# Kernel tuning notes

Measured on AMD Instinct MI355X. Metric: run time of the kernel, lower is better.

Reference implementation:

```python
import jax, jax.numpy as jnp
import numpy as np

BN_EPS = 1e-5
NN_CHUNK = 1024  # unknown points processed per distance-matrix tile


def _batch_ids(cnt, total):
    # contiguous per-batch layout -> batch id of each point via cumsum/searchsorted
    return jnp.searchsorted(jnp.cumsum(cnt), jnp.arange(total), side='right')


def three_nn(unknown, known, ub_id, kb_id):
    """Ragged brute-force 3-NN. Returns (squared dists [N,3], global idx [N,3])."""
    N = unknown.shape[0]
    nchunk = N // NN_CHUNK
    u = unknown.reshape(nchunk, NN_CHUNK, 3)
    ub = ub_id.reshape(nchunk, NN_CHUNK)

    def body(args):
        uc, bc = args
        d2 = jnp.sum((uc[:, None, :] - known[None, :, :]) ** 2, axis=-1)  # [chunk, M]
        d2 = jnp.where(bc[:, None] == kb_id[None, :], d2, jnp.inf)  # mask cross-batch pairs
        neg_d, idx = jax.lax.top_k(-d2, 3)
        return -neg_d, idx

    d2, idx = jax.lax.map(body, (u, ub))
    return d2.reshape(N, 3), idx.reshape(N, 3)


def three_interpolate(known_feats, idx, weight):
    # gather [N,3,C] then inverse-distance weighted sum -> [N,C]
    gathered = known_feats[idx]  # [N,3,C]
    return jnp.einsum('nkc,nk->nc', gathered, weight)


def conv_bn_relu(x, W, gamma, beta):
    # 1x1 Conv2d over [1,C,N,1] == pointwise matmul; BN (training stats) over points
    h = x @ W.T  # [N, C_out]
    mean = jnp.mean(h, axis=0)
    var = jnp.mean((h - mean) ** 2, axis=0)  # biased, as torch BN normalization
    h = (h - mean) * jax.lax.rsqrt(var + BN_EPS) * gamma + beta
    return jax.nn.relu(h)


def setup_inputs() -> dict:
    key = jax.random.key(0)
    ks = jax.random.split(key, 10)
    B, Nper, Mper, C1, C2 = 4, 16384, 4096, 128, 256
    N, M = B * Nper, B * Mper
    unknown = jax.random.normal(ks[0], (N, 3), jnp.float32) * 10.0
    known = jax.random.normal(ks[1], (M, 3), jnp.float32) * 10.0
    unknown_feats = jax.random.normal(ks[2], (N, C1), jnp.float32)
    known_feats = jax.random.normal(ks[3], (M, C2), jnp.float32)
    unknown_batch_cnt = jnp.full((B,), Nper, jnp.int32)
    known_batch_cnt = jnp.full((B,), Mper, jnp.int32)
    Cin = C1 + C2  # 384
    W1 = jax.random.normal(ks[4], (256, Cin), jnp.float32) * (1.0 / np.sqrt(Cin))
    W2 = jax.random.normal(ks[5], (256, 256), jnp.float32) * (1.0 / np.sqrt(256))
    g1 = jnp.ones((256,), jnp.float32); b1 = jnp.zeros((256,), jnp.float32)
    g2 = jnp.ones((256,), jnp.float32); b2 = jnp.zeros((256,), jnp.float32)
    return {"unknown": unknown, "unknown_batch_cnt": unknown_batch_cnt,
            "known": known, "known_batch_cnt": known_batch_cnt,
            "unknown_feats": unknown_feats, "known_feats": known_feats,
            "W1": W1, "g1": g1, "b1": b1, "W2": W2, "g2": g2, "b2": b2}


def reference(unknown, unknown_batch_cnt, known, known_batch_cnt,
              unknown_feats, known_feats, W1, g1, b1, W2, g2, b2):
    ub_id = _batch_ids(unknown_batch_cnt, unknown.shape[0])
    kb_id = _batch_ids(known_batch_cnt, known.shape[0])
    dist, idx = three_nn(unknown, known, ub_id, kb_id)  # squared dists, as CUDA kernel
    dist_recip = 1.0 / (dist + 1e-8)
    weight = dist_recip / jnp.sum(dist_recip, axis=-1, keepdims=True)
    interpolated = three_interpolate(known_feats, idx, weight)  # [N, C2]
    new_features = jnp.concatenate([interpolated, unknown_feats], axis=1)  # [N, C2+C1]
    new_features = conv_bn_relu(new_features, W1, g1, b1)
    new_features = conv_bn_relu(new_features, W2, g2, b2)
    return new_features  # [N, 256]
```

## Files before the change

kernel.cpp:

```cpp
#include <hip/hip_runtime.h>
#include <math.h>

typedef __attribute__((ext_vector_type(8))) short short8;
typedef __attribute__((ext_vector_type(4))) float f32x4;

#define INF 3.0e38f
#define BN_EPS 1e-5f

#define NB 1024
#define XMIN (-64.0f)
#define BW 0.125f
#define INVW 8.0f
#define PA 192

__device__ __forceinline__ unsigned short f2bf(float x) {
    union { float f; unsigned u; } v; v.f = x;
    unsigned r = v.u + 0x7FFF + ((v.u >> 16) & 1);
    return (unsigned short)(r >> 16);
}
__device__ __forceinline__ float bf2f(unsigned short u) {
    return __uint_as_float(((unsigned)u) << 16);
}
__device__ __forceinline__ unsigned long long shflx_u64(unsigned long long v, int m) {
    int lo = __shfl_xor((int)(unsigned)(v & 0xFFFFFFFFULL), m, 64);
    int hi = __shfl_xor((int)(unsigned)(v >> 32), m, 64);
    return ((unsigned long long)(unsigned)hi << 32) | (unsigned)lo;
}

__global__ __launch_bounds__(256) void hist2_kernel(
    const float* __restrict__ kn, const int* __restrict__ kcnt, int M,
    const float* __restrict__ un, const int* __restrict__ ucnt, int N,
    int B, int* __restrict__ kc, int* __restrict__ qc)
{
    int j = blockIdx.x * 256 + threadIdx.x;
    const float* P; const int* C; int* out; int idx;
    if (j < M) { P = kn; C = kcnt; out = kc; idx = j; }
    else { idx = j - M; if (idx >= N) return; P = un; C = ucnt; out = qc; }
    int cum = 0, bb = 0;
    for (int i = 0; i < B; i++) { int c = C[i]; if (idx >= cum) bb = i; cum += c; }
    float x = P[idx * 3];
    int bi = (int)((x - XMIN) * INVW);
    bi = min(max(bi, 0), NB - 1);
    atomicAdd(&out[bb * NB + bi], 1);
}

__global__ __launch_bounds__(1024) void scan2_kernel(
    const int* __restrict__ kc, int* __restrict__ kbs, int* __restrict__ kcur,
    const int* __restrict__ qc, int* __restrict__ qbs, int* __restrict__ qcur,
    int T)
{
    __shared__ int ts[1024];
    const int* cnt = blockIdx.x ? qc : kc;
    int* bs  = blockIdx.x ? qbs : kbs;
    int* cur = blockIdx.x ? qcur : kcur;

    int tid = threadIdx.x;
    int base = tid * 4;
    int v0 = 0, v1 = 0, v2 = 0, v3 = 0;
    if (base + 0 < T) v0 = cnt[base + 0];
    if (base + 1 < T) v1 = cnt[base + 1];
    if (base + 2 < T) v2 = cnt[base + 2];
    if (base + 3 < T) v3 = cnt[base + 3];
    int s = v0 + v1 + v2 + v3;
    ts[tid] = s;
    __syncthreads();
    for (int off = 1; off < 1024; off <<= 1) {
        int t = (tid >= off) ? ts[tid - off] : 0;
        __syncthreads();
        ts[tid] += t;
        __syncthreads();
    }
    int ex = ts[tid] - s;
    if (base + 0 < T) { bs[base + 0] = ex; cur[base + 0] = ex; } ex += v0;
    if (base + 1 < T) { bs[base + 1] = ex; cur[base + 1] = ex; } ex += v1;
    if (base + 2 < T) { bs[base + 2] = ex; cur[base + 2] = ex; } ex += v2;
    if (base + 3 < T) { bs[base + 3] = ex; cur[base + 3] = ex; } ex += v3;
    if (tid == ((T - 1) >> 2)) bs[T] = ts[tid];
}

__global__ __launch_bounds__(256) void scatter2_kernel(
    const float* __restrict__ kn, const int* __restrict__ kcnt, int M,
    const float* __restrict__ un, const int* __restrict__ ucnt, int N,
    int B, int* __restrict__ kcur, float4* __restrict__ kscat,
    int* __restrict__ qcur, float4* __restrict__ qscat)
{
    int j = blockIdx.x * 256 + threadIdx.x;
    const float* P; const int* C; int* cur; float4* out; int idx;
    if (j < M) { P = kn; C = kcnt; cur = kcur; out = kscat; idx = j; }
    else { idx = j - M; if (idx >= N) return; P = un; C = ucnt; cur = qcur; out = qscat; }
    int cum = 0, bb = 0;
    for (int i = 0; i < B; i++) { int c = C[i]; if (idx >= cum) bb = i; cum += c; }
    float x = P[idx * 3], y = P[idx * 3 + 1], z = P[idx * 3 + 2];
    int bi = (int)((x - XMIN) * INVW);
    bi = min(max(bi, 0), NB - 1);
    int pos = atomicAdd(&cur[bb * NB + bi], 1);
    out[pos] = make_float4(x, y, z, __int_as_float(idx));
}

__global__ __launch_bounds__(256) void knn4_kernel(
    const int* __restrict__ ucnt, const int* __restrict__ kbs,
    const float4* __restrict__ qscat, const float4* __restrict__ scat,
    int B, float* __restrict__ wgt, int* __restrict__ idxo)
{
    int tid = threadIdx.x;
    int wv = tid >> 6;
    int lane = tid & 63;
    int qi = lane & 15;
    int r4 = lane >> 4;
    int pbase = blockIdx.x * 64;
    int qpos = pbase + wv * 16 + qi;

    int cum = 0, bb = 0;
    for (int i = 0; i < B; i++) { int c = ucnt[i]; if (pbase >= cum) bb = i; cum += c; }

    float4 qf = qscat[qpos];
    float ux = qf.x, uy = qf.y, uz = qf.z;

    int kst = kbs[bb * NB];
    int ken = kbs[bb * NB + NB];

    int bq = (int)((ux - XMIN) * INVW);
    bq = min(max(bq, 0), NB - 1);
    int sp = kbs[bb * NB + bq];

    int abase = sp - PA / 2;
    if (abase + PA > ken) abase = ken - PA;
    if (abase < kst) abase = kst;
    int aend = min(abase + PA, ken);

    float d0 = INF, d1 = INF, d2v = INF;
    auto upd = [&](float e) {
        float m0 = fmaxf(e, d0), m1 = fmaxf(e, d1);
        d0 = fminf(e, d0); d1 = fminf(m0, d1); d2v = fminf(m1, d2v);
    };
    {
        int alo = abase + r4 * (PA / 4);
        int ahi = min(alo + PA / 4, aend);
        int i = alo;
        for (; i + 4 <= ahi; i += 4) {
            float e[4];
#pragma unroll
            for (int c = 0; c < 4; c++) {
                float4 f = scat[i + c];
                float dx = f.x - ux, dy = f.y - uy, dz = f.z - uz;
                e[c] = __builtin_fmaf(dx, dx, __builtin_fmaf(dy, dy, dz * dz));
            }
#pragma unroll
            for (int c = 0; c < 4; c++) upd(e[c]);
        }
        for (; i < ahi; i++) {
            float4 f = scat[i];
            float dx = f.x - ux, dy = f.y - uy, dz = f.z - uz;
            upd(__builtin_fmaf(dx, dx, __builtin_fmaf(dy, dy, dz * dz)));
        }
    }
#pragma unroll
    for (int s = 16; s <= 32; s <<= 1) {
        float e0 = __shfl_xor(d0, s, 64);
        float e1 = __shfl_xor(d1, s, 64);
        float e2 = __shfl_xor(d2v, s, 64);
        upd(e0); upd(e1); upd(e2);
    }
    float thr = d2v;

    float Wr = fminf(sqrtf(thr), 300.0f);
    int blo = max((int)((ux - Wr - XMIN) * INVW) - 1, 0);
    int bhi = min((int)((ux + Wr - XMIN) * INVW) + 1, NB - 1);
    int pLo = kbs[bb * NB + blo];
    int pHi = kbs[bb * NB + bhi + 1];
    int n = pHi - pLo;
    int quar = (n + 3) >> 2;
    int mylo = pLo + r4 * quar;
    int myhi = min(mylo + quar, pHi);

    unsigned long long k0 = ~0ULL, k1 = ~0ULL, k2 = ~0ULL;
    auto insK = [&](unsigned long long k) {
        bool cc0 = k < k0;
        unsigned long long t0 = cc0 ? k : k0;
        unsigned long long t1 = cc0 ? k0 : k;
        bool cc1 = t1 < k1;
        unsigned long long u0 = cc1 ? t1 : k1;
        unsigned long long u1 = cc1 ? k1 : t1;
        k0 = t0; k1 = u0;
        k2 = u1 < k2 ? u1 : k2;
    };

    int i = mylo;
    for (; i + 4 <= myhi; i += 4) {
        float e[4]; int ix[4];
#pragma unroll
        for (int c = 0; c < 4; c++) {
            float4 f = scat[i + c];
            float dx = f.x - ux, dy = f.y - uy, dz = f.z - uz;
            e[c] = __builtin_fmaf(dx, dx, __builtin_fmaf(dy, dy, dz * dz));
            ix[c] = __float_as_int(f.w);
        }
        float m4 = fminf(fminf(e[0], e[1]), fminf(e[2], e[3]));
        if (m4 <= thr) {
#pragma unroll
            for (int c = 0; c < 4; c++) {
                if (e[c] <= thr) {
                    insK(((unsigned long long)__float_as_uint(e[c]) << 32) |
                         (unsigned)ix[c]);
                    thr = fminf(thr, __uint_as_float((unsigned)(k2 >> 32)));
                }
            }
        }
    }
    for (; i < myhi; i++) {
        float4 f = scat[i];
        float dx = f.x - ux, dy = f.y - uy, dz = f.z - uz;
        float e = __builtin_fmaf(dx, dx, __builtin_fmaf(dy, dy, dz * dz));
        if (e <= thr) {
            insK(((unsigned long long)__float_as_uint(e) << 32) |
                 (unsigned)__float_as_int(f.w));
            thr = fminf(thr, __uint_as_float((unsigned)(k2 >> 32)));
        }
    }

#pragma unroll
    for (int s = 16; s <= 32; s <<= 1) {
        unsigned long long e0 = shflx_u64(k0, s);
        unsigned long long e1 = shflx_u64(k1, s);
        unsigned long long e2 = shflx_u64(k2, s);
        insK(e0); insK(e1); insK(e2);
    }

    if (r4 == 0) {
        float dd0 = __uint_as_float((unsigned)(k0 >> 32));
        float dd1 = __uint_as_float((unsigned)(k1 >> 32));
        float dd2 = __uint_as_float((unsigned)(k2 >> 32));
        float r0 = 1.0f / (dd0 + 1e-8f);
        float r1 = 1.0f / (dd1 + 1e-8f);
        float r2 = 1.0f / (dd2 + 1e-8f);
        float rs = 1.0f / (r0 + r1 + r2);
        int orig = __float_as_int(qf.w);
        wgt[orig * 3 + 0] = r0 * rs;
        wgt[orig * 3 + 1] = r1 * rs;
        wgt[orig * 3 + 2] = r2 * rs;
        idxo[orig * 3 + 0] = (int)(unsigned)k0;
        idxo[orig * 3 + 1] = (int)(unsigned)k1;
        idxo[orig * 3 + 2] = (int)(unsigned)k2;
    }
}

__global__ __launch_bounds__(256) void wconv_kernel(
    const float* __restrict__ W1, const float* __restrict__ W2,
    unsigned short* __restrict__ W1b, unsigned short* __restrict__ W2b,
    int n1, int n2)
{
    int i = blockIdx.x * 256 + threadIdx.x;
    if (i < n1) W1b[i] = f2bf(W1[i]);
    int j = i - n1;
    if (j >= 0 && j < n2) W2b[j] = f2bf(W2[j]);
}

template <int K, int MODE>
__global__ __launch_bounds__(256) void gemm_bf16_kernel(
    const void* __restrict__ Aa, const float* __restrict__ ufeat,
    const unsigned short* __restrict__ W,
    const float* __restrict__ wgt, const int* __restrict__ idxv,
    const float* __restrict__ bnsum, const float* __restrict__ bnsq,
    const float* __restrict__ bng, const float* __restrict__ bnb, float invN,
    void* __restrict__ Cv, float* __restrict__ gsum, float* __restrict__ gsq)
{
    __shared__ unsigned short As[128 * 40];
    __shared__ unsigned short Bs[128 * 40];
    __shared__ float colsum[128];
    __shared__ float colsq[128];
    __shared__ float sc[256], sh[256];

    int tid = threadIdx.x;
    int w = tid >> 6, lane = tid & 63;
    int r = w >> 1, cq = w & 1;
    int m16 = lane & 15, q = lane >> 4;
    int bm = blockIdx.x * 128, bn = blockIdx.y * 128;

    if (MODE == 1) {
        float mean = bnsum[tid] * invN;
        float var = bnsq[tid] * invN - mean * mean;
        float scv = bng[tid] * rsqrtf(var + BN_EPS);
        sc[tid] = scv;
        sh[tid] = bnb[tid] - mean * scv;
    }

    int srow = tid >> 2;
    int kc = (tid & 3) * 8;
    float w0a[2], w1a[2], w2a[2];
    int j0a[2], j1a[2], j2a[2];
    if (MODE == 2) {
#pragma unroll
        for (int t = 0; t < 2; t++) {
            int pp = bm + srow + 64 * t;
            w0a[t] = wgt[pp * 3 + 0]; w1a[t] = wgt[pp * 3 + 1]; w2a[t] = wgt[pp * 3 + 2];
            j0a[t] = idxv[pp * 3 + 0]; j1a[t] = idxv[pp * 3 + 1]; j2a[t] = idxv[pp * 3 + 2];
        }
    }

    f32x4 acc[4][4];
#pragma unroll
    for (int i = 0; i < 4; i++)
#pragma unroll
        for (int j = 0; j < 4; j++) acc[i][j] = (f32x4){0.f, 0.f, 0.f, 0.f};

#pragma unroll
    for (int k0 = 0; k0 < K; k0 += 32) {
        __syncthreads();
#pragma unroll
        for (int t = 0; t < 2; t++) {
            int row = srow + 64 * t;
            int c = k0 + kc;
            ushort4 o0, o1;
            if (MODE == 2) {
                if (c < 256) {
                    const float* f0 = (const float*)Aa + (size_t)j0a[t] * 256 + c;
                    const float* f1 = (const float*)Aa + (size_t)j1a[t] * 256 + c;
                    const float* f2 = (const float*)Aa + (size_t)j2a[t] * 256 + c;
                    float4 x0 = *(const float4*)f0, x1 = *(const float4*)(f0 + 4);
                    float4 y0 = *(const float4*)f1, y1 = *(const float4*)(f1 + 4);
                    float4 z0 = *(const float4*)f2, z1 = *(const float4*)(f2 + 4);
                    float W0 = w0a[t], W1 = w1a[t], W2 = w2a[t];
                    o0.x = f2bf(x0.x * W0 + y0.x * W1 + z0.x * W2);
                    o0.y = f2bf(x0.y * W0 + y0.y * W1 + z0.y * W2);
                    o0.z = f2bf(x0.z * W0 + y0.z * W1 + z0.z * W2);
                    o0.w = f2bf(x0.w * W0 + y0.w * W1 + z0.w * W2);
                    o1.x = f2bf(x1.x * W0 + y1.x * W1 + z1.x * W2);
                    o1.y = f2bf(x1.y * W0 + y1.y * W1 + z1.y * W2);
                    o1.z = f2bf(x1.z * W0 + y1.z * W1 + z1.z * W2);
                    o1.w = f2bf(x1.w * W0 + y1.w * W1 + z1.w * W2);
                } else {
                    const float* fu = ufeat + (size_t)(bm + row) * 128 + (c - 256);
                    float4 u0 = *(const float4*)fu, u1 = *(const float4*)(fu + 4);
                    o0.x = f2bf(u0.x); o0.y = f2bf(u0.y);
                    o0.z = f2bf(u0.z); o0.w = f2bf(u0.w);
                    o1.x = f2bf(u1.x); o1.y = f2bf(u1.y);
                    o1.z = f2bf(u1.z); o1.w = f2bf(u1.w);
                }
            } else {
                const unsigned short* Ab = (const unsigned short*)Aa;
                ushort4 h0 = *(const ushort4*)(Ab + (size_t)(bm + row) * K + c);
                ushort4 h1v = *(const ushort4*)(Ab + (size_t)(bm + row) * K + c + 4);
                float4 s0 = *(const float4*)&sc[c];
                float4 s1 = *(const float4*)&sc[c + 4];
                float4 t0 = *(const float4*)&sh[c];
                float4 t1 = *(const float4*)&sh[c + 4];
                o0.x = f2bf(fmaxf(bf2f(h0.x) * s0.x + t0.x, 0.f));
                o0.y = f2bf(fmaxf(bf2f(h0.y) * s0.y + t0.y, 0.f));
                o0.z = f2bf(fmaxf(bf2f(h0.z) * s0.z + t0.z, 0.f));
                o0.w = f2bf(fmaxf(bf2f(h0.w) * s0.w + t0.w, 0.f));
                o1.x = f2bf(fmaxf(bf2f(h1v.x) * s1.x + t1.x, 0.f));
                o1.y = f2bf(fmaxf(bf2f(h1v.y) * s1.y + t1.y, 0.f));
                o1.z = f2bf(fmaxf(bf2f(h1v.z) * s1.z + t1.z, 0.f));
                o1.w = f2bf(fmaxf(bf2f(h1v.w) * s1.w + t1.w, 0.f));
            }
            *(ushort4*)&As[row * 40 + kc] = o0;
            *(ushort4*)&As[row * 40 + kc + 4] = o1;
            *(short8*)&Bs[row * 40 + kc] =
                *(const short8*)(W + (size_t)(bn + row) * K + k0 + kc);
        }
        __syncthreads();

        short8 af[4], bf[4];
#pragma unroll
        for (int sub = 0; sub < 4; sub++) {
            af[sub] = *(const short8*)&As[(r * 64 + sub * 16 + m16) * 40 + q * 8];
            bf[sub] = *(const short8*)&Bs[(cq * 64 + sub * 16 + m16) * 40 + q * 8];
        }
#pragma unroll
        for (int sm = 0; sm < 4; sm++)
#pragma unroll
            for (int sn = 0; sn < 4; sn++)
                acc[sm][sn] = __builtin_amdgcn_mfma_f32_16x16x32_bf16(
                    af[sm], bf[sn], acc[sm][sn], 0, 0, 0);
    }

    int row0 = bm + r * 64 + q * 4;
    int col0 = bn + cq * 64 + m16;
#pragma unroll
    for (int sm = 0; sm < 4; sm++)
#pragma unroll
        for (int sn = 0; sn < 4; sn++) {
            f32x4 v = acc[sm][sn];
#pragma unroll
            for (int reg = 0; reg < 4; reg++) {
                size_t idx = (size_t)(row0 + sm * 16 + reg) * 256 + col0 + sn * 16;
                if (MODE == 2) ((unsigned short*)Cv)[idx] = f2bf(v[reg]);
                else           ((float*)Cv)[idx] = v[reg];
            }
        }

    __syncthreads();
    if (tid < 128) { colsum[tid] = 0.f; colsq[tid] = 0.f; }
    __syncthreads();
#pragma unroll
    for (int sn = 0; sn < 4; sn++) {
        float sacc = 0.f, qacc = 0.f;
#pragma unroll
        for (int sm = 0; sm < 4; sm++) {
            f32x4 v = acc[sm][sn];
#pragma unroll
            for (int reg = 0; reg < 4; reg++) {
                sacc += v[reg];
                qacc += v[reg] * v[reg];
            }
        }
        int lc = cq * 64 + sn * 16 + m16;
        atomicAdd(&colsum[lc], sacc);
        atomicAdd(&colsq[lc], qacc);
    }
    __syncthreads();
    if (tid < 128) {
        atomicAdd(&gsum[bn + tid], colsum[tid]);
        atomicAdd(&gsq[bn + tid], colsq[tid]);
    }
}

__global__ __launch_bounds__(256) void final_act_kernel(
    const float* __restrict__ h2, const float* __restrict__ bnsum,
    const float* __restrict__ bnsq, const float* __restrict__ bng,
    const float* __restrict__ bnb, float invN,
    float* __restrict__ out, int total4)
{
    __shared__ float sc[256], sh[256];
    int c = threadIdx.x;
    float mean = bnsum[c] * invN;
    float var = bnsq[c] * invN - mean * mean;
    float scv = bng[c] * rsqrtf(var + BN_EPS);
    sc[c] = scv;
    sh[c] = bnb[c] - mean * scv;
    __syncthreads();

    int i = blockIdx.x * 256 + threadIdx.x;
    if (i >= total4) return;
    int c4 = i & 63;
    float4 v = ((const float4*)h2)[i];
    float4 s = *(const float4*)&sc[c4 * 4];
    float4 t = *(const float4*)&sh[c4 * 4];
    float4 o;
    o.x = fmaxf(v.x * s.x + t.x, 0.0f);
    o.y = fmaxf(v.y * s.y + t.y, 0.0f);
    o.z = fmaxf(v.z * s.z + t.z, 0.0f);
    o.w = fmaxf(v.w * s.w + t.w, 0.0f);
    ((float4*)out)[i] = o;
}

extern "C" void kernel_launch(void* const* d_in, const int* in_sizes, int n_in,
                              void* d_out, int out_size, void* d_ws, size_t ws_size,
                              hipStream_t stream)
{
    const float* unknown = (const float*)d_in[0];
    const int*   ucnt    = (const int*)d_in[1];
    const float* known   = (const float*)d_in[2];
    const int*   kcnt    = (const int*)d_in[3];
    const float* ufeat   = (const float*)d_in[4];
    const float* kfeat   = (const float*)d_in[5];
    const float* W1      = (const float*)d_in[6];
    const float* g1      = (const float*)d_in[7];
    const float* b1      = (const float*)d_in[8];
    const float* W2      = (const float*)d_in[9];
    const float* g2      = (const float*)d_in[10];
    const float* b2      = (const float*)d_in[11];

    int N = in_sizes[0] / 3;
    int B = in_sizes[1];
    int M = in_sizes[2] / 3;
    int T = B * NB;

    char* ws = (char*)d_ws;
    size_t off = 0;
    float* wgt = (float*)(ws + off);            off += (size_t)N * 3 * 4;
    int*   idxb = (int*)(ws + off);             off += (size_t)N * 3 * 4;
    float* stats = (float*)(ws + off);          off += 4 * 256 * 4;
    float* sum1 = stats,        *sq1 = stats + 256;
    float* sum2 = stats + 512,  *sq2 = stats + 768;
    int* kch = (int*)(ws + off);                off += (size_t)T * 4;
    int* qch = (int*)(ws + off);                off += (size_t)T * 4;
    int* kbs = (int*)(ws + off);                off += ((size_t)T + 1) * 4;
    int* qbs = (int*)(ws + off);                off += ((size_t)T + 1) * 4;
    int* kcur = (int*)(ws + off);               off += (size_t)T * 4;
    int* qcur = (int*)(ws + off);               off += (size_t)T * 4;
    unsigned short* W1b = (unsigned short*)(ws + off);  off += 256 * 384 * 2;
    unsigned short* W2b = (unsigned short*)(ws + off);  off += 256 * 256 * 2;
    off = (off + 255) & ~(size_t)255;
    float4* kscat = (float4*)(ws + off);        off += (size_t)M * sizeof(float4);
    float4* qscat = (float4*)(ws + off);        off += (size_t)N * sizeof(float4);
    off = (off + 255) & ~(size_t)255;
    unsigned short* h1 = (unsigned short*)(ws + off);   off += (size_t)N * 256 * 2;
    off = (off + 255) & ~(size_t)255;
    float* h2 = (float*)(ws + off);

    float invN = 1.0f / (float)N;

    hipMemsetAsync(stats, 0, 4 * 256 * 4 + 2 * (size_t)T * 4, stream);

    wconv_kernel<<<(256 * 384 + 256 * 256 + 255) / 256, 256, 0, stream>>>(
        W1, W2, W1b, W2b, 256 * 384, 256 * 256);

    hist2_kernel<<<(M + N + 255) / 256, 256, 0, stream>>>(
        known, kcnt, M, unknown, ucnt, N, B, kch, qch);
    scan2_kernel<<<2, 1024, 0, stream>>>(kch, kbs, kcur, qch, qbs, qcur, T);
    scatter2_kernel<<<(M + N + 255) / 256, 256, 0, stream>>>(
        known, kcnt, M, unknown, ucnt, N, B, kcur, kscat, qcur, qscat);
    knn4_kernel<<<N / 64, 256, 0, stream>>>(ucnt, kbs, qscat, kscat,
                                            B, wgt, idxb);

    gemm_bf16_kernel<384, 2><<<dim3(N / 128, 2), 256, 0, stream>>>(
        kfeat, ufeat, W1b, wgt, idxb,
        nullptr, nullptr, nullptr, nullptr, 0.f, h1, sum1, sq1);
    gemm_bf16_kernel<256, 1><<<dim3(N / 128, 2), 256, 0, stream>>>(
        h1, nullptr, W2b, nullptr, nullptr,
        sum1, sq1, g1, b1, invN, h2, sum2, sq2);
    final_act_kernel<<<N / 4, 256, 0, stream>>>(h2, sum2, sq2, g2, b2, invN,
                                                (float*)d_out, N * 64);
}
```

Baseline: 416.6 us.

## Stage candidate known points in shared memory for block-wide KNN search

The KNN kernel now loads the initial candidate window once per block into LDS, centred on a representative query of the block and widened to 256 points. It then computes the union of all queries' slab ranges and streams that range through LDS in 1024-point chunks, so the 64 queries in a block share each load instead of each thread reading global memory. The trade-off is extra block barriers, and every query now walks the chunk loop over the whole block union even when its own range is narrower. The shared initial window may also give a looser starting threshold for queries far from the block centre.

```diff
diff --git a/kernel.cpp b/kernel.cpp
--- a/kernel.cpp
+++ b/kernel.cpp
@@ -11,7 +11,8 @@
 #define XMIN (-64.0f)
 #define BW 0.125f
 #define INVW 8.0f
-#define PA 192
+#define PA 256
+#define CH 1024
 
 __device__ __forceinline__ unsigned short f2bf(float x) {
     union { float f; unsigned u; } v; v.f = x;
@@ -97,11 +98,14 @@
     out[pos] = make_float4(x, y, z, __int_as_float(idx));
 }
 
-__global__ __launch_bounds__(256) void knn4_kernel(
+__global__ __launch_bounds__(256) void knn5_kernel(
     const int* __restrict__ ucnt, const int* __restrict__ kbs,
     const float4* __restrict__ qscat, const float4* __restrict__ scat,
     int B, float* __restrict__ wgt, int* __restrict__ idxo)
 {
+    __shared__ float4 cs[CH];
+    __shared__ int ured[8];
+
     int tid = threadIdx.x;
     int wv = tid >> 6;
     int lane = tid & 63;
@@ -119,40 +123,27 @@
     int kst = kbs[bb * NB];
     int ken = kbs[bb * NB + NB];
 
-    int bq = (int)((ux - XMIN) * INVW);
+    float cx = qscat[pbase + 32].x;
+    int bq = (int)((cx - XMIN) * INVW);
     bq = min(max(bq, 0), NB - 1);
     int sp = kbs[bb * NB + bq];
-
     int abase = sp - PA / 2;
     if (abase + PA > ken) abase = ken - PA;
     if (abase < kst) abase = kst;
-    int aend = min(abase + PA, ken);
+    int alen = min(abase + PA, ken) - abase;
+
+    for (int i = tid; i < alen; i += 256) cs[i] = scat[abase + i];
+    __syncthreads();
 
     float d0 = INF, d1 = INF, d2v = INF;
     auto upd = [&](float e) {
         float m0 = fmaxf(e, d0), m1 = fmaxf(e, d1);
         d0 = fminf(e, d0); d1 = fminf(m0, d1); d2v = fminf(m1, d2v);
     };
-    {
-        int alo = abase + r4 * (PA / 4);
-        int ahi = min(alo + PA / 4, aend);
-        int i = alo;
-        for (; i + 4 <= ahi; i += 4) {
-            float e[4];
-#pragma unroll
-            for (int c = 0; c < 4; c++) {
-                float4 f = scat[i + c];
-                float dx = f.x - ux, dy = f.y - uy, dz = f.z - uz;
-                e[c] = __builtin_fmaf(dx, dx, __builtin_fmaf(dy, dy, dz * dz));
-            }
-#pragma unroll
-            for (int c = 0; c < 4; c++) upd(e[c]);
-        }
-        for (; i < ahi; i++) {
-            float4 f = scat[i];
-            float dx = f.x - ux, dy = f.y - uy, dz = f.z - uz;
-            upd(__builtin_fmaf(dx, dx, __builtin_fmaf(dy, dy, dz * dz)));
-        }
+    for (int i = r4; i < alen; i += 4) {
+        float4 f = cs[i];
+        float dx = f.x - ux, dy = f.y - uy, dz = f.z - uz;
+        upd(__builtin_fmaf(dx, dx, __builtin_fmaf(dy, dy, dz * dz)));
     }
 #pragma unroll
     for (int s = 16; s <= 32; s <<= 1) {
@@ -172,6 +163,17 @@
     int quar = (n + 3) >> 2;
     int mylo = pLo + r4 * quar;
     int myhi = min(mylo + quar, pHi);
+
+    int wlo = pLo, whi = pHi;
+#pragma unroll
+    for (int s = 1; s < 64; s <<= 1) {
+        wlo = min(wlo, __shfl_xor(wlo, s, 64));
+        whi = max(whi, __shfl_xor(whi, s, 64));
+    }
+    if (lane == 0) { ured[wv] = wlo; ured[4 + wv] = whi; }
+    __syncthreads();
+    int uLo = min(min(ured[0], ured[1]), min(ured[2], ured[3]));
+    int uHi = max(max(ured[4], ured[5]), max(ured[6], ured[7]));
 
     unsigned long long k0 = ~0ULL, k1 = ~0ULL, k2 = ~0ULL;
     auto insK = [&](unsigned long long k) {
@@ -185,36 +187,45 @@
         k2 = u1 < k2 ? u1 : k2;
     };
 
-    int i = mylo;
-    for (; i + 4 <= myhi; i += 4) {
-        float e[4]; int ix[4];
-#pragma unroll
-        for (int c = 0; c < 4; c++) {
-            float4 f = scat[i + c];
-            float dx = f.x - ux, dy = f.y - uy, dz = f.z - uz;
-            e[c] = __builtin_fmaf(dx, dx, __builtin_fmaf(dy, dy, dz * dz));
-            ix[c] = __float_as_int(f.w);
-        }
-        float m4 = fminf(fminf(e[0], e[1]), fminf(e[2], e[3]));
-        if (m4 <= thr) {
+    for (int cb = uLo; cb < uHi; cb += CH) {
+        int ce = min(cb + CH, uHi);
+        int clen = ce - cb;
+        __syncthreads();
+        for (int i = tid; i < clen; i += 256) cs[i] = scat[cb + i];
+        __syncthreads();
+
+        int lo = max(mylo, cb), hi = min(myhi, ce);
+        int i = lo;
+        for (; i + 4 <= hi; i += 4) {
+            float e[4]; int ix[4];
 #pragma unroll
             for (int c = 0; c < 4; c++) {
-                if (e[c] <= thr) {
-                    insK(((unsigned long long)__float_as_uint(e[c]) << 32) |
-                         (unsigned)ix[c]);
-                    thr = fminf(thr, __uint_as_float((unsigned)(k2 >> 32)));
+                float4 f = cs[i - cb + c];
+                float dx = f.x - ux, dy = f.y - uy, dz = f.z - uz;
+                e[c] = __builtin_fmaf(dx, dx, __builtin_fmaf(dy, dy, dz * dz));
+                ix[c] = __float_as_int(f.w);
+            }
+            float m4 = fminf(fminf(e[0], e[1]), fminf(e[2], e[3]));
+            if (m4 <= thr) {
+#pragma unroll
+                for (int c = 0; c < 4; c++) {
+                    if (e[c] <= thr) {
+                        insK(((unsigned long long)__float_as_uint(e[c]) << 32) |
+                             (unsigned)ix[c]);
+                        thr = fminf(thr, __uint_as_float((unsigned)(k2 >> 32)));
+                    }
                 }
             }
         }
-    }
-    for (; i < myhi; i++) {
-        float4 f = scat[i];
-        float dx = f.x - ux, dy = f.y - uy, dz = f.z - uz;
-        float e = __builtin_fmaf(dx, dx, __builtin_fmaf(dy, dy, dz * dz));
-        if (e <= thr) {
-            insK(((unsigned long long)__float_as_uint(e) << 32) |
-                 (unsigned)__float_as_int(f.w));
-            thr = fminf(thr, __uint_as_float((unsigned)(k2 >> 32)));
+        for (; i < hi; i++) {
+            float4 f = cs[i - cb];
+            float dx = f.x - ux, dy = f.y - uy, dz = f.z - uz;
+            float e = __builtin_fmaf(dx, dx, __builtin_fmaf(dy, dy, dz * dz));
+            if (e <= thr) {
+                insK(((unsigned long long)__float_as_uint(e) << 32) |
+                     (unsigned)__float_as_int(f.w));
+                thr = fminf(thr, __uint_as_float((unsigned)(k2 >> 32)));
+            }
         }
     }
 
@@ -501,7 +512,7 @@
     scan2_kernel<<<2, 1024, 0, stream>>>(kch, kbs, kcur, qch, qbs, qcur, T);
     scatter2_kernel<<<(M + N + 255) / 256, 256, 0, stream>>>(
         known, kcnt, M, unknown, ucnt, N, B, kcur, kscat, qcur, qscat);
-    knn4_kernel<<<N / 64, 256, 0, stream>>>(ucnt, kbs, qscat, kscat,
+    knn5_kernel<<<N / 64, 256, 0, stream>>>(ucnt, kbs, qscat, kscat,
                                             B, wgt, idxb);
 
     gemm_bf16_kernel<384, 2><<<dim3(N / 128, 2), 256, 0, stream>>>(
```

Result: slower. 472.8 us (+13.5%).
